# Performance work log

Hardware: AMD Instinct MI355X
Metric: run time of the kernel (lower is better)

The kernel has to match this reference:

```python
import jax, jax.numpy as jnp
import numpy as np

B, L, D, P = 8, 2048, 1024, 256


def _ln(x):
    # LayerNorm without scale/offset (haiku default eps=1e-5)
    m = x.mean(-1, keepdims=True)
    v = x.var(-1, keepdims=True)
    return (x - m) * jax.lax.rsqrt(v + 1e-5)


def _s5(u, Lam_re, Lam_im, B_re, B_im, C_re, C_im, D_diag, log_step):
    # S5 diagonal SSM, ZOH discretization, parallel associative scan.
    Lam = Lam_re + 1j * Lam_im                      # (P,)
    dt = jnp.exp(log_step)                          # (P,)
    Lam_bar = jnp.exp(Lam * dt)                     # (P,)
    Bc = B_re + 1j * B_im                           # (P, D)
    B_bar = ((Lam_bar - 1.0) / Lam)[:, None] * Bc   # (P, D)
    Bu = jnp.einsum('bld,pd->blp', u.astype(B_bar.dtype), B_bar)  # (B, L, P)
    A = jnp.broadcast_to(Lam_bar, Bu.shape)

    def binop(e1, e2):
        a1, b1 = e1
        a2, b2 = e2
        return a1 * a2, a2 * b1 + b2

    _, xs = jax.lax.associative_scan(binop, (A, Bu), axis=1)  # (B, L, P)
    Cc = C_re + 1j * C_im                            # (D, P)
    return 2.0 * jnp.einsum('blp,dp->bld', xs, Cc).real + D_diag * u


def setup_inputs() -> dict:
    key = jax.random.key(0)
    ks = jax.random.split(key, 16)
    inp = {
        'y': jax.random.normal(ks[0], (B, L, D), jnp.float32),
        't': jax.random.normal(ks[1], (B, D), jnp.float32),
        # modulation projection m: Linear(D -> 6D)  (random instead of zero-init so output is non-trivial)
        'Wm': jax.random.normal(ks[2], (D, 6 * D), jnp.float32) * 0.02,
        'bm': jax.random.normal(ks[3], (6 * D,), jnp.float32) * 0.02,
        # S5Dual params
        'Lam_re': -0.5 * jnp.ones((P,), jnp.float32),
        'Lam_im': jnp.pi * jnp.arange(P, dtype=jnp.float32),
        'B_re': jax.random.normal(ks[4], (P, D), jnp.float32) / np.sqrt(D),
        'B_im': jax.random.normal(ks[5], (P, D), jnp.float32) / np.sqrt(D),
        'C_re': jax.random.normal(ks[6], (D, P), jnp.float32) / np.sqrt(P),
        'C_im': jax.random.normal(ks[7], (D, P), jnp.float32) / np.sqrt(P),
        'D_diag': jax.random.normal(ks[8], (D,), jnp.float32),
        'log_step': jax.random.uniform(ks[9], (P,), jnp.float32,
                                       np.log(0.001), np.log(0.1)),
        # AdaLN (norm2) projection: Linear(D -> 2D)
        'Wc': jax.random.normal(ks[10], (D, 2 * D), jnp.float32) * 0.02,
        'bc': jax.random.normal(ks[11], (2 * D,), jnp.float32) * 0.02,
        # FeedForward: pre Linear(D -> 4D), pos Linear(4D -> D) (random instead of zero-init)
        'W1': jax.random.normal(ks[12], (D, 4 * D), jnp.float32) / np.sqrt(D),
        'b1': jnp.zeros((4 * D,), jnp.float32),
        'W2': jax.random.normal(ks[13], (4 * D, D), jnp.float32) / np.sqrt(4 * D) * 0.1,
        'b2': jnp.zeros((D,), jnp.float32),
    }
    return inp


def reference(y, t, Wm, bm, Lam_re, Lam_im, B_re, B_im, C_re, C_im,
              D_diag, log_step, Wc, bc, W1, b1, W2, b2):
    # m(t) -> 6-way split
    mod = t @ Wm + bm
    shift_a, scale_a, gate_a, shift_ff, scale_ff, gate_ff = jnp.split(mod, 6, axis=-1)

    # S5 block with AdaLN-style modulation
    y_mod = _ln(y) * (1 + scale_a[:, None]) + shift_a[:, None]
    a_y = _s5(y_mod, Lam_re, Lam_im, B_re, B_im, C_re, C_im, D_diag, log_step)
    y = y + gate_a[:, None] * a_y

    # FFN block: norm2 is AdaLN(cond=t) composed with modulate(shift_ff, scale_ff)
    cond = t @ Wc + bc
    scale_c, shift_c = jnp.split(cond, 2, axis=-1)
    y_norm = _ln(y) * (1 + scale_c[:, None]) + shift_c[:, None]
    y_mod = y_norm * (1 + scale_ff[:, None]) + shift_ff[:, None]
    h = jax.nn.gelu(y_mod @ W1 + b1)
    ff_y = h @ W2 + b2
    return y + gate_ff[:, None] * ff_y
```

## Files before the change

### kernel.cpp

```cpp
#include <hip/hip_runtime.h>
#include <hip/hip_bf16.h>

#define Bsz 8
#define Lseq 2048
#define Dm 1024
#define Pst 256
#define BL (Bsz*Lseq)

typedef short bf16x8 __attribute__((ext_vector_type(8)));
typedef float f32x4  __attribute__((ext_vector_type(4)));

__device__ __forceinline__ float4 ldg4(const float* p){ return *reinterpret_cast<const float4*>(p); }
__device__ __forceinline__ ushort f2bf(float f){
    __hip_bfloat16 h = __float2bfloat16(f);
    return *reinterpret_cast<ushort*>(&h);
}
__device__ __forceinline__ float bf2f(ushort u){
    __hip_bfloat16 h = *reinterpret_cast<__hip_bfloat16*>(&u);
    return __bfloat162float(h);
}

__global__ __launch_bounds__(256) void proj2_k(
    const float* __restrict__ T, const float* __restrict__ W,
    const float* __restrict__ bias, float* __restrict__ Out, int N)
{
    __shared__ float ts[8][128];
    int j = blockIdx.x*256 + threadIdx.x;
    int d0 = blockIdx.y*128;
    for (int i = threadIdx.x; i < 8*128; i += 256) {
        int b = i >> 7, d = i & 127;
        ts[b][d] = T[(size_t)b*Dm + d0 + d];
    }
    __syncthreads();
    float acc[8] = {};
    #pragma unroll 4
    for (int d = 0; d < 128; ++d) {
        float w = W[(size_t)(d0 + d)*N + j];
        #pragma unroll
        for (int b = 0; b < 8; ++b) acc[b] += ts[b][d]*w;
    }
    float bv = (blockIdx.y == 0) ? bias[j] : 0.f;
    #pragma unroll
    for (int b = 0; b < 8; ++b)
        atomicAdd(&Out[(size_t)b*N + j], acc[b] + bv);
}

__global__ __launch_bounds__(256) void ssm_setup_k(
    const float* __restrict__ Lam_re, const float* __restrict__ Lam_im,
    const float* __restrict__ B_re, const float* __restrict__ B_im,
    const float* __restrict__ log_step, float* __restrict__ lam, ushort* __restrict__ Bbar_bf)
{
    int p = blockIdx.x;
    float lr = Lam_re[p], li = Lam_im[p];
    float dt = expf(log_step[p]);
    float e  = expf(lr*dt);
    float cr = e * cosf(li*dt);
    float ci = e * sinf(li*dt);
    float d2 = lr*lr + li*li;
    float nr = cr - 1.0f, ni = ci;
    float gr = (nr*lr + ni*li) / d2;
    float gi = (ni*lr - nr*li) / d2;
    if (threadIdx.x == 0) { lam[2*p] = cr; lam[2*p+1] = ci; }
    for (int d = threadIdx.x; d < Dm; d += 256) {
        float br = B_re[(size_t)p*Dm + d], bi = B_im[(size_t)p*Dm + d];
        Bbar_bf[(size_t)p*Dm + d]         = f2bf(gr*br - gi*bi);
        Bbar_bf[(size_t)(Pst+p)*Dm + d]   = f2bf(gr*bi + gi*br);
    }
}

__global__ __launch_bounds__(256) void ccat_k(
    const float* __restrict__ C_re, const float* __restrict__ C_im, ushort* __restrict__ Ccat_bf)
{
    int d = blockIdx.x;
    int p = threadIdx.x;
    Ccat_bf[(size_t)d*(2*Pst) + p]       = f2bf( 2.0f*C_re[(size_t)d*Pst + p]);
    Ccat_bf[(size_t)d*(2*Pst) + Pst + p] = f2bf(-2.0f*C_im[(size_t)d*Pst + p]);
}

__global__ __launch_bounds__(256) void transp_k(
    const float* __restrict__ in, ushort* __restrict__ out, int R, int C)
{
    __shared__ float tile[32][33];
    int tx = threadIdx.x & 31, ty = threadIdx.x >> 5;
    int r0 = blockIdx.y*32, c0 = blockIdx.x*32;
    #pragma unroll
    for (int j = 0; j < 4; ++j)
        tile[ty + j*8][tx] = in[(size_t)(r0 + ty + j*8)*C + c0 + tx];
    __syncthreads();
    #pragma unroll
    for (int j = 0; j < 4; ++j)
        out[(size_t)(c0 + ty + j*8)*R + r0 + tx] = f2bf(tile[tx][ty + j*8]);
}

template<int MODE>
__global__ __launch_bounds__(256) void ln_mod_k(
    const float* __restrict__ X, ushort* __restrict__ Y,
    const float* __restrict__ mod, const float* __restrict__ cond)
{
    int row = blockIdx.x;
    int b = row >> 11;
    int t = threadIdx.x;
    const float* xr = X + (size_t)row*Dm;
    float4 v = ldg4(xr + t*4);
    float s  = v.x + v.y + v.z + v.w;
    float ss = v.x*v.x + v.y*v.y + v.z*v.z + v.w*v.w;
    #pragma unroll
    for (int o = 32; o > 0; o >>= 1) { s += __shfl_down(s, o); ss += __shfl_down(ss, o); }
    __shared__ float red[8];
    int wid = t >> 6;
    if ((t & 63) == 0) { red[wid] = s; red[4+wid] = ss; }
    __syncthreads();
    float S  = red[0]+red[1]+red[2]+red[3];
    float SS = red[4]+red[5]+red[6]+red[7];
    float mean = S * (1.0f/Dm);
    float var  = SS * (1.0f/Dm) - mean*mean;
    float rstd = rsqrtf(var + 1e-5f);
    int d0 = t*4;
    float xv[4] = {v.x, v.y, v.z, v.w};
    ushort o4[4];
    #pragma unroll
    for (int q = 0; q < 4; ++q) {
        int d = d0 + q;
        float ln = (xv[q] - mean) * rstd;
        float r;
        if (MODE == 0) {
            r = ln * (1.0f + mod[(size_t)b*6144 + 1024 + d]) + mod[(size_t)b*6144 + d];
        } else {
            float yn = ln * (1.0f + cond[(size_t)b*2048 + d]) + cond[(size_t)b*2048 + 1024 + d];
            r = yn * (1.0f + mod[(size_t)b*6144 + 4096 + d]) + mod[(size_t)b*6144 + 3072 + d];
        }
        o4[q] = f2bf(r);
    }
    *reinterpret_cast<ushort4*>(Y + (size_t)row*Dm + d0) =
        make_ushort4(o4[0], o4[1], o4[2], o4[3]);
}

__global__ __launch_bounds__(256) void scan1_k(
    const float* __restrict__ Bu, const float* __restrict__ lam, float* __restrict__ carry)
{
    int bc = blockIdx.x;
    int b = bc >> 5, c = bc & 31;
    int p = threadIdx.x;
    float ar = lam[2*p], ai = lam[2*p+1];
    float xr = 0.f, xi = 0.f;
    const float* base = Bu + ((size_t)(b*Lseq + c*64))*(2*Pst);
    #pragma unroll 4
    for (int i = 0; i < 64; ++i) {
        float br = base[(size_t)i*(2*Pst) + p];
        float bi = base[(size_t)i*(2*Pst) + Pst + p];
        float nxr = ar*xr - ai*xi + br;
        float nxi = ar*xi + ai*xr + bi;
        xr = nxr; xi = nxi;
    }
    carry[((size_t)bc*Pst + p)*2]     = xr;
    carry[((size_t)bc*Pst + p)*2 + 1] = xi;
}

__global__ __launch_bounds__(256) void scan2_k(float* __restrict__ carry, const float* __restrict__ lam)
{
    int b = blockIdx.x;
    int p = threadIdx.x;
    float ar = lam[2*p], ai = lam[2*p+1];
    float pr = ar, pi = ai;
    #pragma unroll
    for (int s = 0; s < 6; ++s) { float nr = pr*pr - pi*pi, ni = 2.f*pr*pi; pr = nr; pi = ni; }
    float sr = 0.f, si = 0.f;
    for (int c = 0; c < 32; ++c) {
        size_t idx = ((size_t)(b*32 + c)*Pst + p)*2;
        float tr = carry[idx], ti = carry[idx+1];
        carry[idx] = sr; carry[idx+1] = si;
        float nr = pr*sr - pi*si + tr;
        float ni = pr*si + pi*sr + ti;
        sr = nr; si = ni;
    }
}

__global__ __launch_bounds__(256) void scan3_k(
    float* __restrict__ Bu, const float* __restrict__ lam, const float* __restrict__ carry)
{
    int bc = blockIdx.x;
    int b = bc >> 5, c = bc & 31;
    int p = threadIdx.x;
    float ar = lam[2*p], ai = lam[2*p+1];
    float xr = carry[((size_t)bc*Pst + p)*2];
    float xi = carry[((size_t)bc*Pst + p)*2 + 1];
    float* base = Bu + ((size_t)(b*Lseq + c*64))*(2*Pst);
    #pragma unroll 4
    for (int i = 0; i < 64; ++i) {
        float br = base[(size_t)i*(2*Pst) + p];
        float bi = base[(size_t)i*(2*Pst) + Pst + p];
        float nxr = ar*xr - ai*xi + br;
        float nxi = ar*xi + ai*xr + bi;
        xr = nxr; xi = nxi;
        base[(size_t)i*(2*Pst) + p] = xr;
        base[(size_t)i*(2*Pst) + Pst + p] = xi;
    }
}

#define BKP 72

template<int EPI, int AFP32>
__global__ __launch_bounds__(256) void gemm_mfma_k(
    const void* __restrict__ Av, const ushort* __restrict__ Bt, float* __restrict__ C,
    int M, int N, int K,
    const float* __restrict__ ep0, const float* __restrict__ ep1,
    const float* __restrict__ ep2, const ushort* __restrict__ ep3u, int m0)
{
    __shared__ ushort As[128*BKP];
    __shared__ ushort Bs[128*BKP];
    int tid = threadIdx.x;
    int nwg = gridDim.x * gridDim.y;
    int lin = blockIdx.y * gridDim.x + blockIdx.x;
    int cpx = nwg >> 3;
    int swz = (lin & 7) * cpx + (lin >> 3);
    int bx = swz % gridDim.x, by = swz / gridDim.x;

    int w = tid >> 6, l = tid & 63;
    int wr = w >> 1, wc = w & 1;
    int lr = l & 15, lk = l >> 4;

    f32x4 acc[4][4];
    #pragma unroll
    for (int i = 0; i < 4; ++i)
        #pragma unroll
        for (int j = 0; j < 4; ++j)
            #pragma unroll
            for (int q = 0; q < 4; ++q) acc[i][j][q] = 0.f;

    const ushort* Ab = (const ushort*)Av;
    const float*  Af = (const float*)Av;

    for (int kt = 0; kt < K; kt += 64) {
        if (AFP32) {
            #pragma unroll
            for (int j = 0; j < 8; ++j) {
                int idx = tid + j*256;
                int r = idx >> 4, f4 = idx & 15;
                float4 v = ldg4(Af + (size_t)(by*128 + r)*K + kt + f4*4);
                *reinterpret_cast<ushort4*>(&As[r*BKP + f4*4]) =
                    make_ushort4(f2bf(v.x), f2bf(v.y), f2bf(v.z), f2bf(v.w));
            }
        } else {
            #pragma unroll
            for (int j = 0; j < 4; ++j) {
                int idx = tid + j*256;
                int r = idx >> 3, kc = idx & 7;
                int4 v = *reinterpret_cast<const int4*>(Ab + (size_t)(by*128 + r)*K + kt + kc*8);
                *reinterpret_cast<int4*>(&As[r*BKP + kc*8]) = v;
            }
        }
        #pragma unroll
        for (int j = 0; j < 4; ++j) {
            int idx = tid + j*256;
            int r = idx >> 3, kc = idx & 7;
            int4 v = *reinterpret_cast<const int4*>(Bt + (size_t)(bx*128 + r)*K + kt + kc*8);
            *reinterpret_cast<int4*>(&Bs[r*BKP + kc*8]) = v;
        }
        __syncthreads();
        #pragma unroll
        for (int mk = 0; mk < 2; ++mk) {
            bf16x8 a[4], b[4];
            #pragma unroll
            for (int mi = 0; mi < 4; ++mi)
                a[mi] = *reinterpret_cast<bf16x8*>(&As[(wr*64 + mi*16 + lr)*BKP + mk*32 + lk*8]);
            #pragma unroll
            for (int ni = 0; ni < 4; ++ni)
                b[ni] = *reinterpret_cast<bf16x8*>(&Bs[(wc*64 + ni*16 + lr)*BKP + mk*32 + lk*8]);
            #pragma unroll
            for (int mi = 0; mi < 4; ++mi)
                #pragma unroll
                for (int ni = 0; ni < 4; ++ni)
                    acc[mi][ni] = __builtin_amdgcn_mfma_f32_16x16x32_bf16(
                        a[mi], b[ni], acc[mi][ni], 0, 0, 0);
        }
        __syncthreads();
    }

    int row0 = by*128 + wr*64;
    int col0 = bx*128 + wc*64;
    #pragma unroll
    for (int mi = 0; mi < 4; ++mi) {
        #pragma unroll
        for (int ni = 0; ni < 4; ++ni) {
            int n = col0 + ni*16 + lr;
            #pragma unroll
            for (int q = 0; q < 4; ++q) {
                int m = row0 + mi*16 + lk*4 + q;
                float v = acc[mi][ni][q];
                if (EPI == 0) {
                    C[(size_t)m*N + n] = v;
                } else if (EPI == 1) {
                    int b = m >> 11;
                    float g  = ep1[(size_t)b*6144 + 2048 + n];
                    float dd = ep2[n];
                    float uu = bf2f(ep3u[(size_t)m*Dm + n]);
                    C[(size_t)m*Dm + n] = ep0[(size_t)m*Dm + n] + g*(v + dd*uu);
                } else if (EPI == 2) {
                    float x = v + ep0[n];
                    float x3 = x*x*x;
                    float r = 0.5f*x*(1.0f + tanhf(0.7978845608028654f*(x + 0.044715f*x3)));
                    ((ushort*)C)[(size_t)m*N + n] = f2bf(r);
                } else {
                    int gm = m0 + m; int b = gm >> 11;
                    float g = ep1[(size_t)b*6144 + 5120 + n];
                    C[(size_t)gm*Dm + n] += g*(v + ep0[n]);
                }
            }
        }
    }
}

extern "C" void kernel_launch(void* const* d_in, const int* in_sizes, int n_in,
                              void* d_out, int out_size, void* d_ws, size_t ws_size,
                              hipStream_t stream) {
    const float* y      = (const float*)d_in[0];
    const float* t      = (const float*)d_in[1];
    const float* Wm     = (const float*)d_in[2];
    const float* bm     = (const float*)d_in[3];
    const float* Lam_re = (const float*)d_in[4];
    const float* Lam_im = (const float*)d_in[5];
    const float* B_re   = (const float*)d_in[6];
    const float* B_im   = (const float*)d_in[7];
    const float* C_re   = (const float*)d_in[8];
    const float* C_im   = (const float*)d_in[9];
    const float* Ddiag  = (const float*)d_in[10];
    const float* lstep  = (const float*)d_in[11];
    const float* Wc     = (const float*)d_in[12];
    const float* bcn    = (const float*)d_in[13];
    const float* W1     = (const float*)d_in[14];
    const float* b1     = (const float*)d_in[15];
    const float* W2     = (const float*)d_in[16];
    const float* b2     = (const float*)d_in[17];
    float* out = (float*)d_out;
    char* ws = (char*)d_ws;

    ushort* u_bf    = (ushort*)ws;
    float*  Bu      = (float*)(ws + (32ull<<20));
    ushort* Bbar_bf = (ushort*)(ws + (64ull<<20));
    ushort* Ccat_bf = (ushort*)(ws + (65ull<<20));
    ushort* W1t     = (ushort*)(ws + (66ull<<20));
    ushort* W2t     = (ushort*)(ws + (74ull<<20));
    float*  mod     = (float*)(ws + (82ull<<20));
    float*  cond    = (float*)(ws + (82ull<<20) + 196608);
    float*  lam     = (float*)(ws + (82ull<<20) + 262144);
    float*  carry   = (float*)(ws + (82ull<<20) + 327680);
    ushort* y2_bf = u_bf;
    ushort* h_bf  = (ushort*)Bu;

    hipMemsetAsync(mod, 0, 262144, stream);
    proj2_k<<<dim3(24,8),256,0,stream>>>(t, Wm, bm, mod, 6144);
    proj2_k<<<dim3(8,8),256,0,stream>>>(t, Wc, bcn, cond, 2048);
    ssm_setup_k<<<256,256,0,stream>>>(Lam_re, Lam_im, B_re, B_im, lstep, lam, Bbar_bf);
    ccat_k<<<1024,256,0,stream>>>(C_re, C_im, Ccat_bf);
    transp_k<<<dim3(128,32),256,0,stream>>>(W1, W1t, 1024, 4096);
    transp_k<<<dim3(32,128),256,0,stream>>>(W2, W2t, 4096, 1024);
    ln_mod_k<0><<<BL,256,0,stream>>>(y, u_bf, mod, nullptr);
    gemm_mfma_k<0,0><<<dim3(4,128),256,0,stream>>>(u_bf, Bbar_bf, Bu, BL, 512, 1024,
                                                   nullptr, nullptr, nullptr, nullptr, 0);
    scan1_k<<<256,256,0,stream>>>(Bu, lam, carry);
    scan2_k<<<8,256,0,stream>>>(carry, lam);
    scan3_k<<<256,256,0,stream>>>(Bu, lam, carry);
    gemm_mfma_k<1,1><<<dim3(8,128),256,0,stream>>>(Bu, Ccat_bf, out, BL, 1024, 512,
                                                   y, mod, Ddiag, u_bf, 0);
    ln_mod_k<1><<<BL,256,0,stream>>>(out, y2_bf, mod, cond);
    for (int mc = 0; mc < 4; ++mc) {
        const ushort* y2c = y2_bf + (size_t)mc*4096*Dm;
        gemm_mfma_k<2,0><<<dim3(32,32),256,0,stream>>>(y2c, W1t, (float*)h_bf, 4096, 4096, 1024,
                                                       b1, nullptr, nullptr, nullptr, 0);
        gemm_mfma_k<3,0><<<dim3(8,32),256,0,stream>>>(h_bf, W2t, out, 4096, 1024, 4096,
                                                      b2, mod, nullptr, nullptr, mc*4096);
    }
}
```

Before: 958.9 us.

## Load GEMM tiles via direct global-to-LDS loads and emit bf16 scan output

The GEMM tile loader now uses global_load_lds builtins that copy 16-byte chunks from global memory straight into shared memory, skipping the round trip through registers. The padded LDS stride of 72 is dropped to 64 to fit the direct-load layout, which may bring back LDS bank conflicts on the MFMA operand reads. The scan's final pass now writes its states as bf16 into a separate buffer, so the C-projection GEMM no longer reads and converts fp32 inputs, and the fp32-A template path is removed.

```diff
diff --git a/kernel.cpp b/kernel.cpp
--- a/kernel.cpp
+++ b/kernel.cpp
@@ -18,6 +18,11 @@
 __device__ __forceinline__ float bf2f(ushort u){
     __hip_bfloat16 h = *reinterpret_cast<__hip_bfloat16*>(&u);
     return __bfloat162float(h);
+}
+__device__ __forceinline__ void gload16(const void* g, void* l) {
+    __builtin_amdgcn_global_load_lds(
+        (const __attribute__((address_space(1))) void*)g,
+        (__attribute__((address_space(3))) void*)l, 16, 0, 0);
 }
 
 __global__ __launch_bounds__(256) void proj2_k(
@@ -176,7 +181,8 @@
 }
 
 __global__ __launch_bounds__(256) void scan3_k(
-    float* __restrict__ Bu, const float* __restrict__ lam, const float* __restrict__ carry)
+    const float* __restrict__ Bu, const float* __restrict__ lam, const float* __restrict__ carry,
+    ushort* __restrict__ xs_bf)
 {
     int bc = blockIdx.x;
     int b = bc >> 5, c = bc & 31;
@@ -184,7 +190,8 @@
     float ar = lam[2*p], ai = lam[2*p+1];
     float xr = carry[((size_t)bc*Pst + p)*2];
     float xi = carry[((size_t)bc*Pst + p)*2 + 1];
-    float* base = Bu + ((size_t)(b*Lseq + c*64))*(2*Pst);
+    const float* base = Bu + ((size_t)(b*Lseq + c*64))*(2*Pst);
+    ushort* obase = xs_bf + ((size_t)(b*Lseq + c*64))*(2*Pst);
     #pragma unroll 4
     for (int i = 0; i < 64; ++i) {
         float br = base[(size_t)i*(2*Pst) + p];
@@ -192,22 +199,20 @@
         float nxr = ar*xr - ai*xi + br;
         float nxi = ar*xi + ai*xr + bi;
         xr = nxr; xi = nxi;
-        base[(size_t)i*(2*Pst) + p] = xr;
-        base[(size_t)i*(2*Pst) + Pst + p] = xi;
-    }
-}
-
-#define BKP 72
-
-template<int EPI, int AFP32>
+        obase[(size_t)i*(2*Pst) + p]       = f2bf(xr);
+        obase[(size_t)i*(2*Pst) + Pst + p] = f2bf(xi);
+    }
+}
+
+template<int EPI>
 __global__ __launch_bounds__(256) void gemm_mfma_k(
-    const void* __restrict__ Av, const ushort* __restrict__ Bt, float* __restrict__ C,
+    const ushort* __restrict__ Ab, const ushort* __restrict__ Bt, float* __restrict__ C,
     int M, int N, int K,
     const float* __restrict__ ep0, const float* __restrict__ ep1,
     const float* __restrict__ ep2, const ushort* __restrict__ ep3u, int m0)
 {
-    __shared__ ushort As[128*BKP];
-    __shared__ ushort Bs[128*BKP];
+    __shared__ ushort As[128*64];
+    __shared__ ushort Bs[128*64];
     int tid = threadIdx.x;
     int nwg = gridDim.x * gridDim.y;
     int lin = blockIdx.y * gridDim.x + blockIdx.x;
@@ -219,6 +224,9 @@
     int wr = w >> 1, wc = w & 1;
     int lr = l & 15, lk = l >> 4;
 
+    int srow = w*32 + (l >> 3);
+    int scol = (l & 7)*8;
+
     f32x4 acc[4][4];
     #pragma unroll
     for (int i = 0; i < 4; ++i)
@@ -227,45 +235,25 @@
             #pragma unroll
             for (int q = 0; q < 4; ++q) acc[i][j][q] = 0.f;
 
-    const ushort* Ab = (const ushort*)Av;
-    const float*  Af = (const float*)Av;
-
     for (int kt = 0; kt < K; kt += 64) {
-        if (AFP32) {
-            #pragma unroll
-            for (int j = 0; j < 8; ++j) {
-                int idx = tid + j*256;
-                int r = idx >> 4, f4 = idx & 15;
-                float4 v = ldg4(Af + (size_t)(by*128 + r)*K + kt + f4*4);
-                *reinterpret_cast<ushort4*>(&As[r*BKP + f4*4]) =
-                    make_ushort4(f2bf(v.x), f2bf(v.y), f2bf(v.z), f2bf(v.w));
-            }
-        } else {
-            #pragma unroll
-            for (int j = 0; j < 4; ++j) {
-                int idx = tid + j*256;
-                int r = idx >> 3, kc = idx & 7;
-                int4 v = *reinterpret_cast<const int4*>(Ab + (size_t)(by*128 + r)*K + kt + kc*8);
-                *reinterpret_cast<int4*>(&As[r*BKP + kc*8]) = v;
-            }
-        }
-        #pragma unroll
-        for (int j = 0; j < 4; ++j) {
-            int idx = tid + j*256;
-            int r = idx >> 3, kc = idx & 7;
-            int4 v = *reinterpret_cast<const int4*>(Bt + (size_t)(bx*128 + r)*K + kt + kc*8);
-            *reinterpret_cast<int4*>(&Bs[r*BKP + kc*8]) = v;
-        }
+        #pragma unroll
+        for (int j = 0; j < 4; ++j)
+            gload16(Ab + (size_t)(by*128 + srow + j*8)*K + kt + scol,
+                    &As[(w*32 + j*8)*64]);
+        #pragma unroll
+        for (int j = 0; j < 4; ++j)
+            gload16(Bt + (size_t)(bx*128 + srow + j*8)*K + kt + scol,
+                    &Bs[(w*32 + j*8)*64]);
         __syncthreads();
         #pragma unroll
         for (int mk = 0; mk < 2; ++mk) {
             bf16x8 a[4], b[4];
             #pragma unroll
             for (int mi = 0; mi < 4; ++mi)
-                a[mi] = *reinterpret_cast<bf16x8*>(&As[(wr*64 + mi*16 + lr)*BKP + mk*32 + lk*8]);
+                a[mi] = *reinterpret_cast<bf16x8*>(&As[(wr*64 + mi*16 + lr)*64 + mk*32 + lk*8]);
             #pragma unroll
             for (int ni = 0; ni < 4; ++ni)
-                b[ni] = *reinterpret_cast<bf16x8*>(&Bs[(wc*64 + ni*16 + lr)*BKP + mk*32 + lk*8]);
+                b[ni] = *reinterpret_cast<bf16x8*>(&Bs[(wc*64 + ni*16 + lr)*64 + mk*32 + lk*8]);
             #pragma unroll
             for (int mi = 0; mi < 4; ++mi)
                 #pragma unroll
@@ -336,14 +324,15 @@
 
     ushort* u_bf    = (ushort*)ws;
     float*  Bu      = (float*)(ws + (32ull<<20));
-    ushort* Bbar_bf = (ushort*)(ws + (64ull<<20));
-    ushort* Ccat_bf = (ushort*)(ws + (65ull<<20));
-    ushort* W1t     = (ushort*)(ws + (66ull<<20));
-    ushort* W2t     = (ushort*)(ws + (74ull<<20));
-    float*  mod     = (float*)(ws + (82ull<<20));
-    float*  cond    = (float*)(ws + (82ull<<20) + 196608);
-    float*  lam     = (float*)(ws + (82ull<<20) + 262144);
-    float*  carry   = (float*)(ws + (82ull<<20) + 327680);
+    ushort* xs_bf   = (ushort*)(ws + (64ull<<20));
+    ushort* Bbar_bf = (ushort*)(ws + (80ull<<20));
+    ushort* Ccat_bf = (ushort*)(ws + (81ull<<20));
+    ushort* W1t     = (ushort*)(ws + (82ull<<20));
+    ushort* W2t     = (ushort*)(ws + (90ull<<20));
+    float*  mod     = (float*)(ws + (98ull<<20));
+    float*  cond    = (float*)(ws + (98ull<<20) + 196608);
+    float*  lam     = (float*)(ws + (98ull<<20) + 262144);
+    float*  carry   = (float*)(ws + (98ull<<20) + 327680);
     ushort* y2_bf = u_bf;
     ushort* h_bf  = (ushort*)Bu;
 
@@ -355,19 +344,19 @@
     transp_k<<<dim3(128,32),256,0,stream>>>(W1, W1t, 1024, 4096);
     transp_k<<<dim3(32,128),256,0,stream>>>(W2, W2t, 4096, 1024);
     ln_mod_k<0><<<BL,256,0,stream>>>(y, u_bf, mod, nullptr);
-    gemm_mfma_k<0,0><<<dim3(4,128),256,0,stream>>>(u_bf, Bbar_bf, Bu, BL, 512, 1024,
-                                                   nullptr, nullptr, nullptr, nullptr, 0);
+    gemm_mfma_k<0><<<dim3(4,128),256,0,stream>>>(u_bf, Bbar_bf, Bu, BL, 512, 1024,
+                                                 nullptr, nullptr, nullptr, nullptr, 0);
     scan1_k<<<256,256,0,stream>>>(Bu, lam, carry);
     scan2_k<<<8,256,0,stream>>>(carry, lam);
-    scan3_k<<<256,256,0,stream>>>(Bu, lam, carry);
-    gemm_mfma_k<1,1><<<dim3(8,128),256,0,stream>>>(Bu, Ccat_bf, out, BL, 1024, 512,
-                                                   y, mod, Ddiag, u_bf, 0);
+    scan3_k<<<256,256,0,stream>>>(Bu, lam, carry, xs_bf);
+    gemm_mfma_k<1><<<dim3(8,128),256,0,stream>>>(xs_bf, Ccat_bf, out, BL, 1024, 512,
+                                                 y, mod, Ddiag, u_bf, 0);
     ln_mod_k<1><<<BL,256,0,stream>>>(out, y2_bf, mod, cond);
     for (int mc = 0; mc < 4; ++mc) {
         const ushort* y2c = y2_bf + (size_t)mc*4096*Dm;
-        gemm_mfma_k<2,0><<<dim3(32,32),256,0,stream>>>(y2c, W1t, (float*)h_bf, 4096, 4096, 1024,
-                                                       b1, nullptr, nullptr, nullptr, 0);
-        gemm_mfma_k<3,0><<<dim3(8,32),256,0,stream>>>(h_bf, W2t, out, 4096, 1024, 4096,
-                                                      b2, mod, nullptr, nullptr, mc*4096);
-    }
-}
+        gemm_mfma_k<2><<<dim3(32,32),256,0,stream>>>(y2c, W1t, (float*)h_bf, 4096, 4096, 1024,
+                                                     b1, nullptr, nullptr, nullptr, 0);
+        gemm_mfma_k<3><<<dim3(8,32),256,0,stream>>>(h_bf, W2t, out, 4096, 1024, 4096,
+                                                    b2, mod, nullptr, nullptr, mc*4096);
+    }
+}
```

Result: slower. 1.043 ms (+8.8%).
